# Kernel tuning notes

Measured on AMD Instinct MI355X. Metric: run time of the kernel, lower is better.

The kernel has to match this reference:

```python
import jax, jax.numpy as jnp
import numpy as np

K = 5  # kensize -> kernel is (2K+1) x (2K+1) = 11x11


def _box_kernels(k):
    r = k
    s = 2 * r + 1
    M13 = np.concatenate([np.ones([r + 1, s]), np.zeros([r, s])], axis=0)  # top half (y1)
    M23 = np.concatenate([np.zeros([r, s]), np.ones([r + 1, s])], axis=0)  # bottom half (y2)
    M11 = np.concatenate([np.ones([s, r + 1]), np.zeros([s, r])], axis=1)  # left half (x1)
    M21 = np.concatenate([np.zeros([s, r]), np.ones([s, r + 1])], axis=1)  # right half (x2)
    to = lambda m: jnp.asarray(m, dtype=jnp.float32).reshape(1, 1, s, s)  # OIHW
    return to(M11), to(M21), to(M13), to(M23)


def setup_inputs() -> dict:
    key = jax.random.key(0)
    x = jax.random.uniform(key, (64, 1, 512, 512), dtype=jnp.float32)
    wx1, wx2, wy1, wy2 = _box_kernels(K)
    return {"x": x, "wx1": wx1, "wx2": wx2, "wy1": wy1, "wy2": wy2}


def _conv(x, w):
    return jax.lax.conv_general_dilated(
        x, w, window_strides=(1, 1), padding="VALID",
        dimension_numbers=("NCHW", "OIHW", "NCHW"))


def reference(x, wx1, wx2, wy1, wy2):
    # reflect-pad by K on H and W, then shift by 0.01 so box sums are > 0
    xp = jnp.pad(x, ((0, 0), (0, 0), (K, K), (K, K)), mode="reflect") + 0.01
    gx1 = _conv(xp, wx1)
    gx2 = _conv(xp, wx2)
    gy1 = _conv(xp, wy1)
    gy2 = _conv(xp, wy2)
    gx = jnp.log(gx1 / gx2)
    gy = jnp.log(gy1 / gy2)
    # L2 norm over the stacked (gx, gy) pair -> [B,1,H,W]
    return jnp.sqrt(gx * gx + gy * gy)
```

## Files before the change

### kernel.cpp

```cpp
#include <hip/hip_runtime.h>
#include <hip/hip_fp16.h>


#define N   512
#define SH  88
#define LN2 0.69314718056f

typedef __fp16 h2  __attribute__((ext_vector_type(2)));
typedef __fp16 h4v __attribute__((ext_vector_type(4)));
typedef __fp16 h8v __attribute__((ext_vector_type(8)));

__device__ __forceinline__ float2 f2add(float2 a, float2 b){ return make_float2(a.x+b.x, a.y+b.y); }
__device__ __forceinline__ float2 f2sub(float2 a, float2 b){ return make_float2(a.x-b.x, a.y-b.y); }

__device__ __forceinline__ void load20(const __half* __restrict__ arr, int base, float* __restrict__ t) {
    h8v a = *(const h8v*)(arr + base);
    h8v b = *(const h8v*)(arr + base + 8);
    h4v c = *(const h4v*)(arr + base + 16);
    #pragma unroll
    for (int j = 0; j < 8; ++j) t[j]      = (float)a[j];
    #pragma unroll
    for (int j = 0; j < 8; ++j) t[8 + j]  = (float)b[j];
    #pragma unroll
    for (int j = 0; j < 4; ++j) t[16 + j] = (float)c[j];
}

__global__ __launch_bounds__(256, 6) void boxlog_kernel(
    const float* __restrict__ x, float* __restrict__ out)
{
    __shared__ __align__(16) __half S6A [69*SH];
    __shared__ __align__(16) __half fulA[64*SH];

    const int tid = threadIdx.x;
    const int wg  = blockIdx.x;
    const int sw  = (wg & 7) * 512 + (wg >> 3);
    const int bz  = sw >> 6;
    const int rem = sw & 63;
    const int by  = rem >> 3;
    const int bx  = rem & 7;
    const int X0 = bx * 64, Y0 = by * 64;
    const float* __restrict__ xb   = x   + (size_t)bz * ((size_t)N * N);
    float* __restrict__       outb = out + (size_t)bz * ((size_t)N * N);

    if (tid < 228) {
        const int rg = tid / 38;
        const int ch = tid - rg * 38;
        const int f0 = rg * 11;
        const int gc = X0 - 6 + 2 * ch;

        auto body = [&](auto loadrow, auto NF, auto NS) {
            constexpr int nf = decltype(NF)::value;
            constexpr int ns = decltype(NS)::value;
            float2 t[21];
            #pragma unroll
            for (int j = 0; j < 11; ++j) t[j] = loadrow(j);
            float2 lo = f2add(f2add(f2add(t[0],t[1]), f2add(t[2],t[3])), f2add(t[4],t[5]));
            float2 hi = f2add(f2add(f2add(t[5],t[6]), f2add(t[7],t[8])), f2add(t[9],t[10]));
            {
                const int b = f0 * SH + 2 * ch;
                float2 fu = f2sub(f2add(lo, hi), t[5]);
                *(h2*)&S6A [b] = __builtin_amdgcn_cvt_pkrtz(lo.x + 0.06f, lo.y + 0.06f);
                *(h2*)&fulA[b] = __builtin_amdgcn_cvt_pkrtz(fu.x + 0.11f, fu.y + 0.11f);
            }
            #pragma unroll
            for (int k = 1; k < ns; ++k) {
                if (k < nf) t[k+10] = loadrow(k + 10);
                lo = f2sub(f2add(lo, t[k+5]), t[k-1]);
                const int b = (f0 + k) * SH + 2 * ch;
                *(h2*)&S6A[b] = __builtin_amdgcn_cvt_pkrtz(lo.x + 0.06f, lo.y + 0.06f);
                if (k < nf) {
                    hi = f2sub(f2add(hi, t[k+10]), t[k+4]);
                    float2 fu = f2sub(f2add(lo, hi), t[k+5]);
                    *(h2*)&fulA[b] = __builtin_amdgcn_cvt_pkrtz(fu.x + 0.11f, fu.y + 0.11f);
                }
            }
        };

        if (by >= 1 && by <= 6 && bx >= 1 && bx <= 6) {
            auto lr = [&](int j) {
                return *(const float2*)(xb + (size_t)(Y0 - 5 + f0 + j) * N + gc);
            };
            if (rg < 5) body(lr, std::integral_constant<int,11>{}, std::integral_constant<int,11>{});
            else        body(lr, std::integral_constant<int, 9>{}, std::integral_constant<int,14>{});
        } else {
            const bool vec = (gc >= 0) && (gc <= N - 2);
            auto lr = [&](int j) {
                int gr = Y0 - 5 + f0 + j;
                gr = gr < 0 ? -gr : (gr > N-1 ? 2*(N-1) - gr : gr);
                const float* rowp = xb + (size_t)gr * N;
                if (vec) return *(const float2*)(rowp + gc);
                int c0 = gc, c1 = gc + 1;
                c0 = c0 < 0 ? -c0 : (c0 > N-1 ? 2*(N-1) - c0 : c0);
                c1 = c1 < 0 ? -c1 : (c1 > N-1 ? 2*(N-1) - c1 : c1);
                return make_float2(rowp[c0], rowp[c1]);
            };
            if (rg < 5) body(lr, std::integral_constant<int,11>{}, std::integral_constant<int,11>{});
            else        body(lr, std::integral_constant<int, 9>{}, std::integral_constant<int,14>{});
        }
    }
    __syncthreads();

    const int tx = tid & 7;
    const int ty = tid >> 3;
    #pragma unroll
    for (int s = 0; s < 2; ++s) {
        const int row  = ty + 32 * s;
        const int base = row * SH + 8 * tx;

        float gy1[8], ly[8];
        {
            float t[20];
            load20(S6A, base, t);
            float g = ((t[1]+t[2])+(t[3]+t[4]))+((t[5]+t[6])+(t[7]+t[8]))+((t[9]+t[10])+t[11]);
            gy1[0] = g;
            #pragma unroll
            for (int p = 1; p < 8; ++p) { g += t[p+11] - t[p]; gy1[p] = g; }
        }
        {
            float t[20];
            load20(S6A, base + 5*SH, t);
            float g = ((t[1]+t[2])+(t[3]+t[4]))+((t[5]+t[6])+(t[7]+t[8]))+((t[9]+t[10])+t[11]);
            ly[0] = __builtin_amdgcn_logf(gy1[0]) - __builtin_amdgcn_logf(g);
            #pragma unroll
            for (int p = 1; p < 8; ++p) {
                g += t[p+11] - t[p];
                ly[p] = __builtin_amdgcn_logf(gy1[p]) - __builtin_amdgcn_logf(g);
            }
        }
        {
            float t[20];
            load20(fulA, base, t);
            float g1 = ((t[1]+t[2])+(t[3]+t[4]))+(t[5]+t[6]);
            float g2 = ((t[6]+t[7])+(t[8]+t[9]))+(t[10]+t[11]);
            float r8[8];
            #pragma unroll
            for (int p = 0; p < 8; ++p) {
                if (p) {
                    g1 += t[p+6]  - t[p];
                    g2 += t[p+11] - t[p+5];
                }
                float lx = __builtin_amdgcn_logf(g1) - __builtin_amdgcn_logf(g2);
                r8[p] = LN2 * __builtin_amdgcn_sqrtf(lx*lx + ly[p]*ly[p]);
            }
            float* op = outb + (size_t)(Y0 + row) * N + X0 + tx * 8;
            *(float4*)op       = make_float4(r8[0], r8[1], r8[2], r8[3]);
            *(float4*)(op + 4) = make_float4(r8[4], r8[5], r8[6], r8[7]);
        }
    }
}

extern "C" void kernel_launch(void* const* d_in, const int* in_sizes, int n_in,
                              void* d_out, int out_size, void* d_ws, size_t ws_size,
                              hipStream_t stream) {
    const float* x = (const float*)d_in[0];
    float* out = (float*)d_out;
    dim3 grid(8 * 8 * 64);
    dim3 block(256);
    boxlog_kernel<<<grid, block, 0, stream>>>(x, out);
}
```

Measured before the change: 34.87 us.

## Shrink tiles to 64x16 with single-wavefront workgroups

Replaces the 64x64 tile, 256-thread workgroup with a 64x16 tile handled by one 64-lane wavefront. 38 lanes build the vertical running sums, each over 26 input rows, and the shared-memory row stride drops from 88 to 80 halves. The grid grows fourfold. The aim is more resident workgroups and less __syncthreads cost across waves. In exchange, the 10-row vertical halo is re-read for every 16 output rows instead of every 64, so more global loads are repeated per output.

```diff
diff --git a/kernel.cpp b/kernel.cpp
--- a/kernel.cpp
+++ b/kernel.cpp
@@ -3,7 +3,7 @@
 
 
 #define N   512
-#define SH  88
+#define SH  80
 #define LN2 0.69314718056f
 
 typedef __fp16 h2  __attribute__((ext_vector_type(2)));
@@ -25,67 +25,58 @@
     for (int j = 0; j < 4; ++j) t[16 + j] = (float)c[j];
 }
 
-__global__ __launch_bounds__(256, 6) void boxlog_kernel(
+__global__ __launch_bounds__(64, 6) void boxlog_kernel(
     const float* __restrict__ x, float* __restrict__ out)
 {
-    __shared__ __align__(16) __half S6A [69*SH];
-    __shared__ __align__(16) __half fulA[64*SH];
+    __shared__ __align__(16) __half S6A [21*SH];
+    __shared__ __align__(16) __half fulA[16*SH];
 
-    const int tid = threadIdx.x;
+    const int lane = threadIdx.x;
     const int wg  = blockIdx.x;
-    const int sw  = (wg & 7) * 512 + (wg >> 3);
-    const int bz  = sw >> 6;
-    const int rem = sw & 63;
+    const int sw  = (wg & 7) * 2048 + (wg >> 3);
+    const int bz  = sw >> 8;
+    const int rem = sw & 255;
     const int by  = rem >> 3;
     const int bx  = rem & 7;
-    const int X0 = bx * 64, Y0 = by * 64;
+    const int X0 = bx * 64, Y0 = by * 16;
     const float* __restrict__ xb   = x   + (size_t)bz * ((size_t)N * N);
     float* __restrict__       outb = out + (size_t)bz * ((size_t)N * N);
 
-    if (tid < 228) {
-        const int rg = tid / 38;
-        const int ch = tid - rg * 38;
-        const int f0 = rg * 11;
-        const int gc = X0 - 6 + 2 * ch;
+    if (lane < 38) {
+        const int gc = X0 - 6 + 2 * lane;
 
-        auto body = [&](auto loadrow, auto NF, auto NS) {
-            constexpr int nf = decltype(NF)::value;
-            constexpr int ns = decltype(NS)::value;
-            float2 t[21];
+        auto body = [&](auto loadrow) {
+            float2 t[26];
             #pragma unroll
             for (int j = 0; j < 11; ++j) t[j] = loadrow(j);
             float2 lo = f2add(f2add(f2add(t[0],t[1]), f2add(t[2],t[3])), f2add(t[4],t[5]));
             float2 hi = f2add(f2add(f2add(t[5],t[6]), f2add(t[7],t[8])), f2add(t[9],t[10]));
             {
-                const int b = f0 * SH + 2 * ch;
                 float2 fu = f2sub(f2add(lo, hi), t[5]);
-                *(h2*)&S6A [b] = __builtin_amdgcn_cvt_pkrtz(lo.x + 0.06f, lo.y + 0.06f);
-                *(h2*)&fulA[b] = __builtin_amdgcn_cvt_pkrtz(fu.x + 0.11f, fu.y + 0.11f);
+                *(h2*)&S6A [2 * lane] = __builtin_amdgcn_cvt_pkrtz(lo.x + 0.06f, lo.y + 0.06f);
+                *(h2*)&fulA[2 * lane] = __builtin_amdgcn_cvt_pkrtz(fu.x + 0.11f, fu.y + 0.11f);
             }
             #pragma unroll
-            for (int k = 1; k < ns; ++k) {
-                if (k < nf) t[k+10] = loadrow(k + 10);
+            for (int k = 1; k < 21; ++k) {
+                if (k < 16) t[k+10] = loadrow(k + 10);
                 lo = f2sub(f2add(lo, t[k+5]), t[k-1]);
-                const int b = (f0 + k) * SH + 2 * ch;
-                *(h2*)&S6A[b] = __builtin_amdgcn_cvt_pkrtz(lo.x + 0.06f, lo.y + 0.06f);
-                if (k < nf) {
+                *(h2*)&S6A[k * SH + 2 * lane] = __builtin_amdgcn_cvt_pkrtz(lo.x + 0.06f, lo.y + 0.06f);
+                if (k < 16) {
                     hi = f2sub(f2add(hi, t[k+10]), t[k+4]);
                     float2 fu = f2sub(f2add(lo, hi), t[k+5]);
-                    *(h2*)&fulA[b] = __builtin_amdgcn_cvt_pkrtz(fu.x + 0.11f, fu.y + 0.11f);
+                    *(h2*)&fulA[k * SH + 2 * lane] = __builtin_amdgcn_cvt_pkrtz(fu.x + 0.11f, fu.y + 0.11f);
                 }
             }
         };
 
-        if (by >= 1 && by <= 6 && bx >= 1 && bx <= 6) {
-            auto lr = [&](int j) {
-                return *(const float2*)(xb + (size_t)(Y0 - 5 + f0 + j) * N + gc);
-            };
-            if (rg < 5) body(lr, std::integral_constant<int,11>{}, std::integral_constant<int,11>{});
-            else        body(lr, std::integral_constant<int, 9>{}, std::integral_constant<int,14>{});
+        if (by >= 1 && by <= 30 && bx >= 1 && bx <= 6) {
+            body([&](int j) {
+                return *(const float2*)(xb + (size_t)(Y0 - 5 + j) * N + gc);
+            });
         } else {
             const bool vec = (gc >= 0) && (gc <= N - 2);
-            auto lr = [&](int j) {
-                int gr = Y0 - 5 + f0 + j;
+            body([&](int j) {
+                int gr = Y0 - 5 + j;
                 gr = gr < 0 ? -gr : (gr > N-1 ? 2*(N-1) - gr : gr);
                 const float* rowp = xb + (size_t)gr * N;
                 if (vec) return *(const float2*)(rowp + gc);
@@ -93,18 +84,16 @@
                 c0 = c0 < 0 ? -c0 : (c0 > N-1 ? 2*(N-1) - c0 : c0);
                 c1 = c1 < 0 ? -c1 : (c1 > N-1 ? 2*(N-1) - c1 : c1);
                 return make_float2(rowp[c0], rowp[c1]);
-            };
-            if (rg < 5) body(lr, std::integral_constant<int,11>{}, std::integral_constant<int,11>{});
-            else        body(lr, std::integral_constant<int, 9>{}, std::integral_constant<int,14>{});
+            });
         }
     }
     __syncthreads();
 
-    const int tx = tid & 7;
-    const int ty = tid >> 3;
+    const int tx = lane & 7;
+    const int ty = lane >> 3;
     #pragma unroll
     for (int s = 0; s < 2; ++s) {
-        const int row  = ty + 32 * s;
+        const int row  = ty + 8 * s;
         const int base = row * SH + 8 * tx;
 
         float gy1[8], ly[8];
@@ -154,7 +143,7 @@
                               hipStream_t stream) {
     const float* x = (const float*)d_in[0];
     float* out = (float*)d_out;
-    dim3 grid(8 * 8 * 64);
-    dim3 block(256);
+    dim3 grid(8 * 32 * 64);
+    dim3 block(64);
     boxlog_kernel<<<grid, block, 0, stream>>>(x, out);
 }
```

Result: faster. 33.30 us, median of 2 (-4.5%).
